# Performance work log

Measured on AMD Instinct MI355X. Metric: run time of the kernel, lower is better.

Reference implementation:

```python
import jax, jax.numpy as jnp
import numpy as np


def setup_inputs() -> dict:
    key = jax.random.key(0)
    ks = jax.random.split(key, 6)
    B, Q, K = 4, 512, 1024
    Dq, Dk, Dv, H = 512, 512, 512, 128
    return {
        "queries": jax.random.normal(ks[0], (B, Q, Dq), dtype=jnp.float32),
        "keys": jax.random.normal(ks[1], (B, K, Dk), dtype=jnp.float32),
        "values": jax.random.normal(ks[2], (B, K, Dv), dtype=jnp.float32),
        "W_q": jax.random.normal(ks[3], (Dq, H), dtype=jnp.float32) / np.sqrt(Dq),
        "W_k": jax.random.normal(ks[4], (Dk, H), dtype=jnp.float32) / np.sqrt(Dk),
        "w_v": jax.random.normal(ks[5], (H,), dtype=jnp.float32) / np.sqrt(H),
    }


def reference(queries, keys, values, W_q, W_k, w_v):
    # Additive (Bahdanau) attention.
    q = jnp.einsum("bqd,dh->bqh", queries, W_q)          # [B,Q,H]
    k = jnp.einsum("bkd,dh->bkh", keys, W_k)             # [B,K,H]
    features = jnp.tanh(q[:, :, None, :] + k[:, None, :, :])  # [B,Q,K,H]
    scores = jnp.einsum("bqkh,h->bqk", features, w_v)    # [B,Q,K]
    attn = jax.nn.softmax(scores, axis=-1)               # [B,Q,K]
    return jnp.einsum("bqk,bkv->bqv", attn, values)      # [B,Q,Dv]
```

## Files before the change

### kernel.cpp

```cpp
#include <hip/hip_runtime.h>

#define BB   4
#define QS   512
#define KSZ  1024
#define DD   512
#define HH   128
#define DVV  512
#define KPN  16

typedef unsigned int uint;
typedef unsigned short ushort;
typedef unsigned long long ull;
typedef __attribute__((ext_vector_type(8)))  short short8;
typedef __attribute__((ext_vector_type(16))) float f32x16;
typedef __attribute__((ext_vector_type(2)))  float f32x2;

__device__ __forceinline__ float rcp_fast(float x)  { return __builtin_amdgcn_rcpf(x); }
__device__ __forceinline__ float exp2_fast(float x) { return __builtin_amdgcn_exp2f(x); }
__device__ __forceinline__ f32x2 lo2(float4 v) { return (f32x2){v.x, v.y}; }
__device__ __forceinline__ f32x2 hi2(float4 v) { return (f32x2){v.z, v.w}; }

__device__ __forceinline__ void split1(float v, ushort& h, ushort& l) {
    uint u = __float_as_uint(v);
    h = (ushort)(u >> 16);
    float r = v - __uint_as_float(u & 0xffff0000u);
    l = (ushort)(__float_as_uint(r) >> 16);
}

__device__ __forceinline__ int hperm(int h) {
    return (h & ~3) | ((h & 1) << 1) | ((h >> 1) & 1);
}

#define NSQ  (BB * QS * DD / 4 / 256)
#define NSK  (BB * KSZ * DD / 4 / 256)
#define NWT  128
#define NPJ  192
#define NVT  (BB * (KSZ / 32) * (DVV / 32))

__global__ __launch_bounds__(256) void split_kernel(
    const float* __restrict__ q, const float* __restrict__ k,
    const float* __restrict__ Wq, const float* __restrict__ Wk,
    const float* __restrict__ wv, float* __restrict__ wvp,
    ushort* __restrict__ qh, ushort* __restrict__ ql,
    ushort* __restrict__ kh, ushort* __restrict__ kl,
    ushort* __restrict__ wqh, ushort* __restrict__ wql,
    ushort* __restrict__ wkh, ushort* __restrict__ wkl)
{
    const int id  = blockIdx.x;
    const int tid = threadIdx.x;

    if (id < NSQ + NSK) {
        const float* src; ushort* dh; ushort* dl; size_t i;
        if (id < NSQ) { src = q; dh = qh; dl = ql; i = (size_t)id * 256 + tid; }
        else          { src = k; dh = kh; dl = kl; i = (size_t)(id - NSQ) * 256 + tid; }
        float4 v = ((const float4*)src)[i];
        ushort h0,h1,h2,h3,l0,l1,l2,l3;
        split1(v.x,h0,l0); split1(v.y,h1,l1); split1(v.z,h2,l2); split1(v.w,h3,l3);
        *(ushort4*)&dh[i * 4] = make_ushort4(h0,h1,h2,h3);
        *(ushort4*)&dl[i * 4] = make_ushort4(l0,l1,l2,l3);
        return;
    }
    __shared__ float Ts[32][33];
    int t = id - (NSQ + NSK);
    if (t == 0 && tid < HH) wvp[hperm(tid)] = wv[tid];
    const float* W; ushort* dh; ushort* dl;
    if (t < 64) { W = Wq; dh = wqh; dl = wql; }
    else        { W = Wk; dh = wkh; dl = wkl; t -= 64; }
    const int d0 = (t >> 2) * 32, h0 = (t & 3) * 32;
    {
        const int dd = tid >> 3, c4 = (tid & 7) * 4;
        float4 v = *(const float4*)&W[(size_t)(d0 + dd) * HH + h0 + c4];
        Ts[dd][c4 + 0] = v.x; Ts[dd][c4 + 1] = v.y;
        Ts[dd][c4 + 2] = v.z; Ts[dd][c4 + 3] = v.w;
    }
    __syncthreads();
    {
        const int hh = tid >> 3, d4 = (tid & 7) * 4;
        ushort h[4], l[4];
        #pragma unroll
        for (int i = 0; i < 4; i++) split1(Ts[d4 + i][hh], h[i], l[i]);
        size_t o = (size_t)(h0 + hh) * DD + d0 + d4;
        *(ushort4*)&dh[o] = make_ushort4(h[0], h[1], h[2], h[3]);
        *(ushort4*)&dl[o] = make_ushort4(l[0], l[1], l[2], l[3]);
    }
}

__global__ __launch_bounds__(256) void projvt_kernel(
    const ushort* __restrict__ qh, const ushort* __restrict__ ql,
    const ushort* __restrict__ kh, const ushort* __restrict__ kl,
    const ushort* __restrict__ wqh, const ushort* __restrict__ wql,
    const ushort* __restrict__ wkh, const ushort* __restrict__ wkl,
    const float* __restrict__ val,
    float* __restrict__ eq, float* __restrict__ ek,
    ushort* __restrict__ vhi, ushort* __restrict__ vlo)
{
    const int id  = blockIdx.x;
    const int tid = threadIdx.x;

    if (id >= NPJ) {
        __shared__ float Ts[32][33];
        const int t   = id - NPJ;
        const int b   = t >> 9;
        const int rem = t & 511;
        const int k0  = (rem >> 4) * 32;
        const int n0  = (rem & 15) * 32;
        {
            const int kk = tid >> 3, n4 = (tid & 7) * 4;
            float4 v = *(const float4*)&val[((size_t)b * KSZ + k0 + kk) * DVV + n0 + n4];
            Ts[kk][n4 + 0] = v.x; Ts[kk][n4 + 1] = v.y;
            Ts[kk][n4 + 2] = v.z; Ts[kk][n4 + 3] = v.w;
        }
        __syncthreads();
        {
            const int nn = tid >> 3, k4 = (tid & 7) * 4;
            ushort h[4], l[4];
            #pragma unroll
            for (int i = 0; i < 4; i++) split1(Ts[k4 + i][nn], h[i], l[i]);
            size_t o = ((size_t)b * DVV + n0 + nn) * KSZ + k0 + k4;
            *(ushort4*)&vhi[o] = make_ushort4(h[0], h[1], h[2], h[3]);
            *(ushort4*)&vlo[o] = make_ushort4(l[0], l[1], l[2], l[3]);
        }
        return;
    }

    const int w = tid >> 6, lane = tid & 63;
    const int row = lane & 31, kg = lane >> 5;
    const int gw = id * 4 + w;

    const ushort *pa_h, *pa_l, *pb_h, *pb_l; float* op; int m0, nt;
    if (gw < 256) {
        m0 = (gw >> 2) * 32; nt = gw & 3;
        pa_h = qh; pa_l = ql; pb_h = wqh; pb_l = wql; op = eq;
    } else {
        const int g = gw - 256;
        m0 = (g >> 2) * 32; nt = g & 3;
        pa_h = kh; pa_l = kl; pb_h = wkh; pb_l = wkl; op = ek;
    }

    const ushort* ah_p = pa_h + (size_t)(m0 + row) * DD + kg * 8;
    const ushort* al_p = pa_l + (size_t)(m0 + row) * DD + kg * 8;
    const ushort* bh_p = pb_h + (size_t)(nt * 32 + row) * DD + kg * 8;
    const ushort* bl_p = pb_l + (size_t)(nt * 32 + row) * DD + kg * 8;

    f32x16 acc;
    #pragma unroll
    for (int i = 0; i < 16; i++) acc[i] = 0.f;

    #pragma unroll 8
    for (int ks = 0; ks < DD; ks += 16) {
        short8 ah = *(const short8*)(ah_p + ks);
        short8 al = *(const short8*)(al_p + ks);
        short8 bh = *(const short8*)(bh_p + ks);
        short8 bl = *(const short8*)(bl_p + ks);
        acc = __builtin_amdgcn_mfma_f32_32x32x16_bf16(ah, bh, acc, 0, 0, 0);
        acc = __builtin_amdgcn_mfma_f32_32x32x16_bf16(ah, bl, acc, 0, 0, 0);
        acc = __builtin_amdgcn_mfma_f32_32x32x16_bf16(al, bh, acc, 0, 0, 0);
    }

    const float C2L = 2.8853900817779268f;
    float* ob = op + (size_t)m0 * HH + nt * 32;
    const int prow = hperm(row);
    #pragma unroll
    for (int r = 0; r < 16; r++) {
        const int rb = (r & 3) + 8 * (r >> 2) + 4 * kg;
        ob[(size_t)rb * HH + prow] = fminf(exp2_fast(acc[r] * C2L), 5.0e4f);
    }
}

__global__ __launch_bounds__(256, 2) void spv_kernel(
    const float* __restrict__ eq, const float* __restrict__ ek,
    const float* __restrict__ wvp,
    const ushort* __restrict__ vhi, const ushort* __restrict__ vlo,
    float* __restrict__ opart, float* __restrict__ rsp)
{
    __shared__ float eqs[64][132];
    __shared__ float eks[64][132];
    ushort (*PhS)[68] = (ushort (*)[68])&eks[0][0];
    ushort (*PlS)[68] = (ushort (*)[68])((ushort*)&eks[0][0] + 64 * 68);

    const int id  = blockIdx.x;
    const int kp  = ((id >> 3) & 1) * 8 + (id & 7);
    const int b   = (id >> 4) & 3;
    const int qt  = id >> 6;

    const int tid  = threadIdx.x;
    const int w    = tid >> 6, lane = tid & 63;
    const int tq   = tid >> 4;
    const int tk   = tid & 15;
    const int wn   = w * 128;
    const int arow = lane & 31;
    const int akg  = lane >> 5;

    const float* eqg = eq + ((size_t)b * QS + qt * 64) * HH;
    const float* ekg = ek + ((size_t)b * KSZ + kp * 64) * HH;
    #pragma unroll
    for (int i = 0; i < 8; i++) {
        int f = tid + i * 256;
        *(float4*)&eqs[f >> 5][(f & 31) * 4] =
            *(const float4*)&eqg[(size_t)(f >> 5) * HH + (f & 31) * 4];
    }
    #pragma unroll
    for (int i = 0; i < 8; i++) {
        int f = tid + i * 256;
        *(float4*)&eks[f >> 5][(f & 31) * 4] =
            *(const float4*)&ekg[(size_t)(f >> 5) * HH + (f & 31) * 4];
    }
    __syncthreads();

    const f32x2 one2 = {1.0f, 1.0f};

#define SGROUP(eq4, ek4, sacc) { \
    f32x2 u02 = __builtin_elementwise_fma(lo2(eq4), lo2(ek4), one2); \
    f32x2 u13 = __builtin_elementwise_fma(hi2(eq4), hi2(ek4), one2); \
    f32x2 p_  = u02 * u13; \
    f32x2 n_  = __builtin_elementwise_fma(wA, u13, wB * u02); \
    float N_  = fmaf(n_.x, p_.y, n_.y * p_.x); \
    sacc = fmaf(N_, rcp_fast(p_.x * p_.y), sacc); }

    float s[4][4];
    #pragma unroll
    for (int a = 0; a < 4; a++)
        #pragma unroll
        for (int c = 0; c < 4; c++) s[a][c] = 0.f;

    #pragma unroll 4
    for (int h = 0; h < HH; h += 4) {
        float4 wp4 = *(const float4*)&wvp[h];
        f32x2 wA = lo2(wp4), wB = hi2(wp4);
        float4 eq4[4], ek4[4];
        #pragma unroll
        for (int a = 0; a < 4; a++) eq4[a] = *(const float4*)&eqs[tq + 16 * a][h];
        #pragma unroll
        for (int c = 0; c < 4; c++) ek4[c] = *(const float4*)&eks[tk + 16 * c][h];
        #pragma unroll
        for (int a = 0; a < 4; a++) {
            #pragma unroll
            for (int c = 0; c < 4; c++) SGROUP(eq4[a], ek4[c], s[a][c]);
        }
    }
#undef SGROUP

    const float CN = -2.8853900817779268f;
    float pv[4][4];
    ushort phv[4][4], plv[4][4];
    float rowacc[4] = {0.f, 0.f, 0.f, 0.f};
    #pragma unroll
    for (int a = 0; a < 4; a++) {
        #pragma unroll
        for (int c = 0; c < 4; c++) {
            pv[a][c] = exp2_fast(s[a][c] * CN);
            split1(pv[a][c], phv[a][c], plv[a][c]);
            rowacc[a] += pv[a][c];
        }
    }

    __syncthreads();

    #pragma unroll
    for (int a = 0; a < 4; a++) {
        #pragma unroll
        for (int c = 0; c < 4; c++) {
            PhS[tq + 16 * a][tk + 16 * c] = phv[a][c];
            PlS[tq + 16 * a][tk + 16 * c] = plv[a][c];
        }
    }

    #pragma unroll
    for (int m = 8; m; m >>= 1) {
        #pragma unroll
        for (int a = 0; a < 4; a++) rowacc[a] += __shfl_xor(rowacc[a], m);
    }
    if (tk == 0) {
        #pragma unroll
        for (int a = 0; a < 4; a++)
            rsp[((size_t)b * QS + qt * 64 + tq + 16 * a) * KPN + kp] = rowacc[a];
    }

    __syncthreads();

    f32x16 acc[2][4];
    #pragma unroll
    for (int hlf = 0; hlf < 2; hlf++)
        #pragma unroll
        for (int nb = 0; nb < 4; nb++)
            #pragma unroll
            for (int i = 0; i < 16; i++) acc[hlf][nb][i] = 0.f;

    const size_t vrow0 = ((size_t)b * DVV + wn + arow) * KSZ + kp * 64 + akg * 8;
    const ushort* vhb = vhi + vrow0;
    const ushort* vlb = vlo + vrow0;

    #pragma unroll
    for (int kb = 0; kb < 4; kb++) {
        short8 ah[2], al[2];
        #pragma unroll
        for (int hlf = 0; hlf < 2; hlf++) {
            { const ull* p = (const ull*)&PhS[hlf * 32 + arow][kb * 16 + akg * 8];
              ((ull*)&ah[hlf])[0] = p[0]; ((ull*)&ah[hlf])[1] = p[1]; }
            { const ull* p = (const ull*)&PlS[hlf * 32 + arow][kb * 16 + akg * 8];
              ((ull*)&al[hlf])[0] = p[0]; ((ull*)&al[hlf])[1] = p[1]; }
        }
        #pragma unroll
        for (int nb = 0; nb < 4; nb++) {
            const size_t o = (size_t)nb * 32 * KSZ + kb * 16;
            short8 vh = *(const short8*)(vhb + o);
            short8 vl = *(const short8*)(vlb + o);
            #pragma unroll
            for (int hlf = 0; hlf < 2; hlf++) {
                acc[hlf][nb] = __builtin_amdgcn_mfma_f32_32x32x16_bf16(ah[hlf], vh, acc[hlf][nb], 0, 0, 0);
                acc[hlf][nb] = __builtin_amdgcn_mfma_f32_32x32x16_bf16(ah[hlf], vl, acc[hlf][nb], 0, 0, 0);
                acc[hlf][nb] = __builtin_amdgcn_mfma_f32_32x32x16_bf16(al[hlf], vh, acc[hlf][nb], 0, 0, 0);
            }
        }
    }

    #pragma unroll
    for (int hlf = 0; hlf < 2; hlf++) {
        float* ob = opart + (((size_t)kp * BB + b) * QS + qt * 64 + hlf * 32) * DVV + wn;
        #pragma unroll
        for (int nb = 0; nb < 4; nb++) {
            #pragma unroll
            for (int r = 0; r < 16; r++) {
                const int rb = (r & 3) + 8 * (r >> 2) + 4 * akg;
                ob[(size_t)rb * DVV + nb * 32 + arow] = acc[hlf][nb][r];
            }
        }
    }
}

__global__ __launch_bounds__(256) void norm_kernel(
    const float* __restrict__ opart, const float* __restrict__ rsp,
    float* __restrict__ outp)
{
    const int i  = blockIdx.x * 256 + threadIdx.x;
    const int n4 = (i & 127) * 4;
    const int q  = (i >> 7) & (QS - 1);
    const int b  = i >> 16;

    const float* rp = rsp + ((size_t)b * QS + q) * KPN;
    float s = 0.f;
    #pragma unroll
    for (int j = 0; j < KPN / 4; j++) {
        float4 r = *(const float4*)(rp + j * 4);
        s += r.x + r.y + r.z + r.w;
    }
    float inv = rcp_fast(s);

    float ox = 0.f, oy = 0.f, oz = 0.f, ow = 0.f;
    #pragma unroll
    for (int kp = 0; kp < KPN; kp++) {
        float4 v = *(const float4*)&opart[(((size_t)kp * BB + b) * QS + q) * DVV + n4];
        ox += v.x; oy += v.y; oz += v.z; ow += v.w;
    }
    float4 res = make_float4(ox * inv, oy * inv, oz * inv, ow * inv);
    *(float4*)&outp[((size_t)b * QS + q) * DVV + n4] = res;
}

extern "C" void kernel_launch(void* const* d_in, const int* in_sizes, int n_in,
                              void* d_out, int out_size, void* d_ws, size_t ws_size,
                              hipStream_t stream)
{
    const float* queries = (const float*)d_in[0];
    const float* keys    = (const float*)d_in[1];
    const float* values  = (const float*)d_in[2];
    const float* Wq      = (const float*)d_in[3];
    const float* Wk      = (const float*)d_in[4];
    const float* wv      = (const float*)d_in[5];
    float* out = (float*)d_out;

    float*  eq    = (float*)d_ws;
    float*  ek    = eq  + (size_t)BB * QS * HH;
    float*  rsp   = ek  + (size_t)BB * KSZ * HH;
    float*  wvp   = rsp + (size_t)BB * QS * KPN;
    float*  opart = wvp + 256;
    ushort* vhi = (ushort*)(opart + (size_t)KPN * BB * QS * DVV);
    ushort* vlo = vhi + (size_t)BB * KSZ * DVV;
    ushort* qh  = vlo + (size_t)BB * KSZ * DVV;
    ushort* ql  = qh  + (size_t)BB * QS * DD;
    ushort* kh  = ql  + (size_t)BB * QS * DD;
    ushort* kl  = kh  + (size_t)BB * KSZ * DD;
    ushort* wqh = kl  + (size_t)BB * KSZ * DD;
    ushort* wql = wqh + (size_t)HH * DD;
    ushort* wkh = wql + (size_t)HH * DD;
    ushort* wkl = wkh + (size_t)HH * DD;

    split_kernel<<<dim3(NSQ + NSK + NWT), 256, 0, stream>>>(
        queries, keys, Wq, Wk, wv, wvp, qh, ql, kh, kl, wqh, wql, wkh, wkl);

    projvt_kernel<<<dim3(NPJ + NVT), 256, 0, stream>>>(
        qh, ql, kh, kl, wqh, wql, wkh, wkl, values, eq, ek, vhi, vlo);

    spv_kernel<<<dim3(512), 256, 0, stream>>>(eq, ek, wvp, vhi, vlo, opart, rsp);

    norm_kernel<<<dim3(1024), 256, 0, stream>>>(opart, rsp, out);
}
```

Before: 147.4 us.

## Halve spv query tile to 32 rows, doubling grid and raising occupancy

The fused score/softmax/PV kernel now processes 32 query rows per block instead of 64. That doubles the grid to 1024 blocks, drops the shared eq tile (queries are read straight from global memory), and raises the launch-bounds occupancy hint from 2 to 4. Each thread computes a 4x2 score tile instead of 4x4, and each wave issues one 32-row MFMA set instead of two. The aim is more waves in flight and less LDS per block. The cost is more global reloads of ek and V, since each V tile is now fetched twice as often, and less work per block over which to amortise loads.

```diff
diff --git a/kernel.cpp b/kernel.cpp
--- a/kernel.cpp
+++ b/kernel.cpp
@@ -167,38 +167,31 @@
     }
 }
 
-__global__ __launch_bounds__(256, 2) void spv_kernel(
+__global__ __launch_bounds__(256, 4) void spv_kernel(
     const float* __restrict__ eq, const float* __restrict__ ek,
     const float* __restrict__ wvp,
     const ushort* __restrict__ vhi, const ushort* __restrict__ vlo,
     float* __restrict__ opart, float* __restrict__ rsp)
 {
-    __shared__ float eqs[64][132];
     __shared__ float eks[64][132];
     ushort (*PhS)[68] = (ushort (*)[68])&eks[0][0];
-    ushort (*PlS)[68] = (ushort (*)[68])((ushort*)&eks[0][0] + 64 * 68);
+    ushort (*PlS)[68] = (ushort (*)[68])((ushort*)&eks[0][0] + 32 * 68);
 
     const int id  = blockIdx.x;
-    const int kp  = ((id >> 3) & 1) * 8 + (id & 7);
+    const int kp  = id & 15;
     const int b   = (id >> 4) & 3;
     const int qt  = id >> 6;
 
     const int tid  = threadIdx.x;
     const int w    = tid >> 6, lane = tid & 63;
-    const int tq   = tid >> 4;
-    const int tk   = tid & 15;
+    const int tq   = tid >> 5;
+    const int tk   = tid & 31;
     const int wn   = w * 128;
     const int arow = lane & 31;
     const int akg  = lane >> 5;
 
-    const float* eqg = eq + ((size_t)b * QS + qt * 64) * HH;
+    const float* eqg = eq + ((size_t)b * QS + qt * 32) * HH;
     const float* ekg = ek + ((size_t)b * KSZ + kp * 64) * HH;
-    #pragma unroll
-    for (int i = 0; i < 8; i++) {
-        int f = tid + i * 256;
-        *(float4*)&eqs[f >> 5][(f & 31) * 4] =
-            *(const float4*)&eqg[(size_t)(f >> 5) * HH + (f & 31) * 4];
-    }
     #pragma unroll
     for (int i = 0; i < 8; i++) {
         int f = tid + i * 256;
@@ -217,74 +210,74 @@
     float N_  = fmaf(n_.x, p_.y, n_.y * p_.x); \
     sacc = fmaf(N_, rcp_fast(p_.x * p_.y), sacc); }
 
-    float s[4][4];
-    #pragma unroll
-    for (int a = 0; a < 4; a++)
-        #pragma unroll
-        for (int c = 0; c < 4; c++) s[a][c] = 0.f;
+    float s[4][2];
+    #pragma unroll
+    for (int a = 0; a < 4; a++) { s[a][0] = 0.f; s[a][1] = 0.f; }
+
+    const float* eqr0 = eqg + (size_t)tq * HH;
+    const float* eqr1 = eqr0 + 8 * HH;
+    const float* eqr2 = eqr0 + 16 * HH;
+    const float* eqr3 = eqr0 + 24 * HH;
 
     #pragma unroll 4
     for (int h = 0; h < HH; h += 4) {
         float4 wp4 = *(const float4*)&wvp[h];
         f32x2 wA = lo2(wp4), wB = hi2(wp4);
-        float4 eq4[4], ek4[4];
-        #pragma unroll
-        for (int a = 0; a < 4; a++) eq4[a] = *(const float4*)&eqs[tq + 16 * a][h];
-        #pragma unroll
-        for (int c = 0; c < 4; c++) ek4[c] = *(const float4*)&eks[tk + 16 * c][h];
+        float4 eq4[4], ek4[2];
+        eq4[0] = *(const float4*)(eqr0 + h);
+        eq4[1] = *(const float4*)(eqr1 + h);
+        eq4[2] = *(const float4*)(eqr2 + h);
+        eq4[3] = *(const float4*)(eqr3 + h);
+        ek4[0] = *(const float4*)&eks[tk][h];
+        ek4[1] = *(const float4*)&eks[tk + 32][h];
         #pragma unroll
         for (int a = 0; a < 4; a++) {
-            #pragma unroll
-            for (int c = 0; c < 4; c++) SGROUP(eq4[a], ek4[c], s[a][c]);
+            SGROUP(eq4[a], ek4[0], s[a][0]);
+            SGROUP(eq4[a], ek4[1], s[a][1]);
         }
     }
 #undef SGROUP
 
     const float CN = -2.8853900817779268f;
-    float pv[4][4];
-    ushort phv[4][4], plv[4][4];
-    float rowacc[4] = {0.f, 0.f, 0.f, 0.f};
+    ushort phv[4][2], plv[4][2];
+    float rowacc[4];
     #pragma unroll
     for (int a = 0; a < 4; a++) {
-        #pragma unroll
-        for (int c = 0; c < 4; c++) {
-            pv[a][c] = exp2_fast(s[a][c] * CN);
-            split1(pv[a][c], phv[a][c], plv[a][c]);
-            rowacc[a] += pv[a][c];
-        }
+        float p0 = exp2_fast(s[a][0] * CN);
+        float p1 = exp2_fast(s[a][1] * CN);
+        split1(p0, phv[a][0], plv[a][0]);
+        split1(p1, phv[a][1], plv[a][1]);
+        rowacc[a] = p0 + p1;
     }
 
     __syncthreads();
 
     #pragma unroll
     for (int a = 0; a < 4; a++) {
-        #pragma unroll
-        for (int c = 0; c < 4; c++) {
-            PhS[tq + 16 * a][tk + 16 * c] = phv[a][c];
-            PlS[tq + 16 * a][tk + 16 * c] = plv[a][c];
-        }
-    }
-
-    #pragma unroll
-    for (int m = 8; m; m >>= 1) {
+        PhS[tq + 8 * a][tk]      = phv[a][0];
+        PlS[tq + 8 * a][tk]      = plv[a][0];
+        PhS[tq + 8 * a][tk + 32] = phv[a][1];
+        PlS[tq + 8 * a][tk + 32] = plv[a][1];
+    }
+
+    #pragma unroll
+    for (int m = 16; m; m >>= 1) {
         #pragma unroll
         for (int a = 0; a < 4; a++) rowacc[a] += __shfl_xor(rowacc[a], m);
     }
     if (tk == 0) {
         #pragma unroll
         for (int a = 0; a < 4; a++)
-            rsp[((size_t)b * QS + qt * 64 + tq + 16 * a) * KPN + kp] = rowacc[a];
+            rsp[((size_t)b * QS + qt * 32 + tq + 8 * a) * KPN + kp] = rowacc[a];
     }
 
     __syncthreads();
 
-    f32x16 acc[2][4];
-    #pragma unroll
-    for (int hlf = 0; hlf < 2; hlf++)
-        #pragma unroll
-        for (int nb = 0; nb < 4; nb++)
-            #pragma unroll
-            for (int i = 0; i < 16; i++) acc[hlf][nb][i] = 0.f;
+    f32x16 acc[4];
+    #pragma unroll
+    for (int nb = 0; nb < 4; nb++)
+        #pragma unroll
+        for (int i = 0; i < 16; i++) acc[nb][i] = 0.f;
 
     const size_t vrow0 = ((size_t)b * DVV + wn + arow) * KSZ + kp * 64 + akg * 8;
     const ushort* vhb = vhi + vrow0;
@@ -292,38 +285,29 @@
 
     #pragma unroll
     for (int kb = 0; kb < 4; kb++) {
-        short8 ah[2], al[2];
-        #pragma unroll
-        for (int hlf = 0; hlf < 2; hlf++) {
-            { const ull* p = (const ull*)&PhS[hlf * 32 + arow][kb * 16 + akg * 8];
-              ((ull*)&ah[hlf])[0] = p[0]; ((ull*)&ah[hlf])[1] = p[1]; }
-            { const ull* p = (const ull*)&PlS[hlf * 32 + arow][kb * 16 + akg * 8];
-              ((ull*)&al[hlf])[0] = p[0]; ((ull*)&al[hlf])[1] = p[1]; }
-        }
+        short8 ah, al;
+        { const ull* p = (const ull*)&PhS[arow][kb * 16 + akg * 8];
+          ((ull*)&ah)[0] = p[0]; ((ull*)&ah)[1] = p[1]; }
+        { const ull* p = (const ull*)&PlS[arow][kb * 16 + akg * 8];
+          ((ull*)&al)[0] = p[0]; ((ull*)&al)[1] = p[1]; }
         #pragma unroll
         for (int nb = 0; nb < 4; nb++) {
             const size_t o = (size_t)nb * 32 * KSZ + kb * 16;
             short8 vh = *(const short8*)(vhb + o);
             short8 vl = *(const short8*)(vlb + o);
-            #pragma unroll
-            for (int hlf = 0; hlf < 2; hlf++) {
-                acc[hlf][nb] = __builtin_amdgcn_mfma_f32_32x32x16_bf16(ah[hlf], vh, acc[hlf][nb], 0, 0, 0);
-                acc[hlf][nb] = __builtin_amdgcn_mfma_f32_32x32x16_bf16(ah[hlf], vl, acc[hlf][nb], 0, 0, 0);
-                acc[hlf][nb] = __builtin_amdgcn_mfma_f32_32x32x16_bf16(al[hlf], vh, acc[hlf][nb], 0, 0, 0);
-            }
-        }
-    }
-
-    #pragma unroll
-    for (int hlf = 0; hlf < 2; hlf++) {
-        float* ob = opart + (((size_t)kp * BB + b) * QS + qt * 64 + hlf * 32) * DVV + wn;
-        #pragma unroll
-        for (int nb = 0; nb < 4; nb++) {
-            #pragma unroll
-            for (int r = 0; r < 16; r++) {
-                const int rb = (r & 3) + 8 * (r >> 2) + 4 * akg;
-                ob[(size_t)rb * DVV + nb * 32 + arow] = acc[hlf][nb][r];
-            }
+            acc[nb] = __builtin_amdgcn_mfma_f32_32x32x16_bf16(ah, vh, acc[nb], 0, 0, 0);
+            acc[nb] = __builtin_amdgcn_mfma_f32_32x32x16_bf16(ah, vl, acc[nb], 0, 0, 0);
+            acc[nb] = __builtin_amdgcn_mfma_f32_32x32x16_bf16(al, vh, acc[nb], 0, 0, 0);
+        }
+    }
+
+    float* ob = opart + (((size_t)kp * BB + b) * QS + qt * 32) * DVV + wn;
+    #pragma unroll
+    for (int nb = 0; nb < 4; nb++) {
+        #pragma unroll
+        for (int r = 0; r < 16; r++) {
+            const int rb = (r & 3) + 8 * (r >> 2) + 4 * akg;
+            ob[(size_t)rb * DVV + nb * 32 + arow] = acc[nb][r];
         }
     }
 }
@@ -390,7 +374,7 @@
     projvt_kernel<<<dim3(NPJ + NVT), 256, 0, stream>>>(
         qh, ql, kh, kl, wqh, wql, wkh, wkl, values, eq, ek, vhi, vlo);
 
-    spv_kernel<<<dim3(512), 256, 0, stream>>>(eq, ek, wvp, vhi, vlo, opart, rsp);
+    spv_kernel<<<dim3(1024), 256, 0, stream>>>(eq, ek, wvp, vhi, vlo, opart, rsp);
 
     norm_kernel<<<dim3(1024), 256, 0, stream>>>(opart, rsp, out);
 }
```

After: 148.3 us. About the same (+0.6%).

## Split score and PV stages, materialize P in bf16 and fuse normalization

Applied to the files above, without the earlier changes.

The fused scores+PV kernel is split into a scores kernel that writes the softmax numerators as hi/lo bf16 planes to global memory, and a PV kernel that computes full-K products per output tile. The split-K partial outputs and the separate normalization pass are removed, and the final reduction and row scaling happen in LDS inside the PV kernel. This trades a large fp32 partial-sum round trip for a smaller bf16 P round trip. V is re-read per q-tile without LDS reuse.

```diff
diff --git a/kernel.cpp b/kernel.cpp
--- a/kernel.cpp
+++ b/kernel.cpp
@@ -167,29 +167,23 @@
     }
 }
 
-__global__ __launch_bounds__(256, 2) void spv_kernel(
+__global__ __launch_bounds__(256, 2) void scores_kernel(
     const float* __restrict__ eq, const float* __restrict__ ek,
     const float* __restrict__ wvp,
-    const ushort* __restrict__ vhi, const ushort* __restrict__ vlo,
-    float* __restrict__ opart, float* __restrict__ rsp)
+    ushort* __restrict__ Phi, ushort* __restrict__ Plo,
+    float* __restrict__ rsp)
 {
     __shared__ float eqs[64][132];
     __shared__ float eks[64][132];
-    ushort (*PhS)[68] = (ushort (*)[68])&eks[0][0];
-    ushort (*PlS)[68] = (ushort (*)[68])((ushort*)&eks[0][0] + 64 * 68);
 
     const int id  = blockIdx.x;
     const int kp  = ((id >> 3) & 1) * 8 + (id & 7);
     const int b   = (id >> 4) & 3;
     const int qt  = id >> 6;
 
-    const int tid  = threadIdx.x;
-    const int w    = tid >> 6, lane = tid & 63;
-    const int tq   = tid >> 4;
-    const int tk   = tid & 15;
-    const int wn   = w * 128;
-    const int arow = lane & 31;
-    const int akg  = lane >> 5;
+    const int tid = threadIdx.x;
+    const int tq  = tid >> 4;
+    const int tk  = tid & 15;
 
     const float* eqg = eq + ((size_t)b * QS + qt * 64) * HH;
     const float* ekg = ek + ((size_t)b * KSZ + kp * 64) * HH;
@@ -241,27 +235,19 @@
 #undef SGROUP
 
     const float CN = -2.8853900817779268f;
-    float pv[4][4];
-    ushort phv[4][4], plv[4][4];
+    ushort* ph = Phi + ((size_t)b * QS + qt * 64) * KSZ + kp * 64;
+    ushort* pl = Plo + ((size_t)b * QS + qt * 64) * KSZ + kp * 64;
     float rowacc[4] = {0.f, 0.f, 0.f, 0.f};
     #pragma unroll
     for (int a = 0; a < 4; a++) {
         #pragma unroll
         for (int c = 0; c < 4; c++) {
-            pv[a][c] = exp2_fast(s[a][c] * CN);
-            split1(pv[a][c], phv[a][c], plv[a][c]);
-            rowacc[a] += pv[a][c];
-        }
-    }
-
-    __syncthreads();
-
-    #pragma unroll
-    for (int a = 0; a < 4; a++) {
-        #pragma unroll
-        for (int c = 0; c < 4; c++) {
-            PhS[tq + 16 * a][tk + 16 * c] = phv[a][c];
-            PlS[tq + 16 * a][tk + 16 * c] = plv[a][c];
+            float p = exp2_fast(s[a][c] * CN);
+            ushort hh, ll;
+            split1(p, hh, ll);
+            size_t o = (size_t)(tq + 16 * a) * KSZ + tk + 16 * c;
+            ph[o] = hh; pl[o] = ll;
+            rowacc[a] += p;
         }
     }
 
@@ -275,85 +261,78 @@
         for (int a = 0; a < 4; a++)
             rsp[((size_t)b * QS + qt * 64 + tq + 16 * a) * KPN + kp] = rowacc[a];
     }
-
+}
+
+__global__ __launch_bounds__(256, 4) void pv_kernel(
+    const ushort* __restrict__ Phi, const ushort* __restrict__ Plo,
+    const ushort* __restrict__ vhi, const ushort* __restrict__ vlo,
+    const float* __restrict__ rsp, float* __restrict__ outp)
+{
+    __shared__ float red[4][32][33];
+    __shared__ float invS[32];
+
+    const int id = blockIdx.x;
+    const int ns = id & 15;
+    const int b  = (id >> 4) & 3;
+    const int qt = id >> 6;
+
+    const int tid = threadIdx.x, w = tid >> 6, lane = tid & 63;
+    const int arow = lane & 31;
+    const int akg  = lane >> 5;
+
+    if (tid < 32) {
+        const float* rp = rsp + ((size_t)b * QS + qt * 32 + tid) * KPN;
+        float s = 0.f;
+        #pragma unroll
+        for (int j = 0; j < KPN / 4; j++) {
+            float4 r = *(const float4*)(rp + j * 4);
+            s += r.x + r.y + r.z + r.w;
+        }
+        invS[tid] = rcp_fast(s);
+    }
+
+    f32x16 acc;
+    #pragma unroll
+    for (int i = 0; i < 16; i++) acc[i] = 0.f;
+
+    const size_t prow = ((size_t)b * QS + qt * 32 + arow) * KSZ + w * 256 + akg * 8;
+    const ushort* php = Phi + prow;
+    const ushort* plp = Plo + prow;
+    const size_t vrow = ((size_t)b * DVV + ns * 32 + arow) * KSZ + w * 256 + akg * 8;
+    const ushort* vhp = vhi + vrow;
+    const ushort* vlp = vlo + vrow;
+
+    #pragma unroll
+    for (int kb = 0; kb < 16; kb++) {
+        const size_t o = (size_t)kb * 16;
+        short8 ah = *(const short8*)(php + o);
+        short8 al = *(const short8*)(plp + o);
+        short8 vh = *(const short8*)(vhp + o);
+        short8 vl = *(const short8*)(vlp + o);
+        acc = __builtin_amdgcn_mfma_f32_32x32x16_bf16(ah, vh, acc, 0, 0, 0);
+        acc = __builtin_amdgcn_mfma_f32_32x32x16_bf16(ah, vl, acc, 0, 0, 0);
+        acc = __builtin_amdgcn_mfma_f32_32x32x16_bf16(al, vh, acc, 0, 0, 0);
+    }
+
+    #pragma unroll
+    for (int r = 0; r < 16; r++) {
+        const int rb = (r & 3) + 8 * (r >> 2) + 4 * akg;
+        red[w][rb][arow] = acc[r];
+    }
     __syncthreads();
 
-    f32x16 acc[2][4];
-    #pragma unroll
-    for (int hlf = 0; hlf < 2; hlf++)
-        #pragma unroll
-        for (int nb = 0; nb < 4; nb++)
-            #pragma unroll
-            for (int i = 0; i < 16; i++) acc[hlf][nb][i] = 0.f;
-
-    const size_t vrow0 = ((size_t)b * DVV + wn + arow) * KSZ + kp * 64 + akg * 8;
-    const ushort* vhb = vhi + vrow0;
-    const ushort* vlb = vlo + vrow0;
-
-    #pragma unroll
-    for (int kb = 0; kb < 4; kb++) {
-        short8 ah[2], al[2];
-        #pragma unroll
-        for (int hlf = 0; hlf < 2; hlf++) {
-            { const ull* p = (const ull*)&PhS[hlf * 32 + arow][kb * 16 + akg * 8];
-              ((ull*)&ah[hlf])[0] = p[0]; ((ull*)&ah[hlf])[1] = p[1]; }
-            { const ull* p = (const ull*)&PlS[hlf * 32 + arow][kb * 16 + akg * 8];
-              ((ull*)&al[hlf])[0] = p[0]; ((ull*)&al[hlf])[1] = p[1]; }
-        }
-        #pragma unroll
-        for (int nb = 0; nb < 4; nb++) {
-            const size_t o = (size_t)nb * 32 * KSZ + kb * 16;
-            short8 vh = *(const short8*)(vhb + o);
-            short8 vl = *(const short8*)(vlb + o);
-            #pragma unroll
-            for (int hlf = 0; hlf < 2; hlf++) {
-                acc[hlf][nb] = __builtin_amdgcn_mfma_f32_32x32x16_bf16(ah[hlf], vh, acc[hlf][nb], 0, 0, 0);
-                acc[hlf][nb] = __builtin_amdgcn_mfma_f32_32x32x16_bf16(ah[hlf], vl, acc[hlf][nb], 0, 0, 0);
-                acc[hlf][nb] = __builtin_amdgcn_mfma_f32_32x32x16_bf16(al[hlf], vh, acc[hlf][nb], 0, 0, 0);
-            }
-        }
-    }
-
-    #pragma unroll
-    for (int hlf = 0; hlf < 2; hlf++) {
-        float* ob = opart + (((size_t)kp * BB + b) * QS + qt * 64 + hlf * 32) * DVV + wn;
-        #pragma unroll
-        for (int nb = 0; nb < 4; nb++) {
-            #pragma unroll
-            for (int r = 0; r < 16; r++) {
-                const int rb = (r & 3) + 8 * (r >> 2) + 4 * akg;
-                ob[(size_t)rb * DVV + nb * 32 + arow] = acc[hlf][nb][r];
-            }
-        }
-    }
-}
-
-__global__ __launch_bounds__(256) void norm_kernel(
-    const float* __restrict__ opart, const float* __restrict__ rsp,
-    float* __restrict__ outp)
-{
-    const int i  = blockIdx.x * 256 + threadIdx.x;
-    const int n4 = (i & 127) * 4;
-    const int q  = (i >> 7) & (QS - 1);
-    const int b  = i >> 16;
-
-    const float* rp = rsp + ((size_t)b * QS + q) * KPN;
-    float s = 0.f;
-    #pragma unroll
-    for (int j = 0; j < KPN / 4; j++) {
-        float4 r = *(const float4*)(rp + j * 4);
-        s += r.x + r.y + r.z + r.w;
-    }
-    float inv = rcp_fast(s);
-
-    float ox = 0.f, oy = 0.f, oz = 0.f, ow = 0.f;
-    #pragma unroll
-    for (int kp = 0; kp < KPN; kp++) {
-        float4 v = *(const float4*)&opart[(((size_t)kp * BB + b) * QS + q) * DVV + n4];
-        ox += v.x; oy += v.y; oz += v.z; ow += v.w;
-    }
-    float4 res = make_float4(ox * inv, oy * inv, oz * inv, ow * inv);
-    *(float4*)&outp[((size_t)b * QS + q) * DVV + n4] = res;
+    const int q  = tid >> 3;
+    const int n4 = (tid & 7) * 4;
+    float4 s0 = *(const float4*)&red[0][q][n4];
+    float4 s1 = *(const float4*)&red[1][q][n4];
+    float4 s2 = *(const float4*)&red[2][q][n4];
+    float4 s3 = *(const float4*)&red[3][q][n4];
+    float inv = invS[q];
+    float4 res = make_float4((s0.x + s1.x + s2.x + s3.x) * inv,
+                             (s0.y + s1.y + s2.y + s3.y) * inv,
+                             (s0.z + s1.z + s2.z + s3.z) * inv,
+                             (s0.w + s1.w + s2.w + s3.w) * inv);
+    *(float4*)&outp[((size_t)b * QS + qt * 32 + q) * DVV + ns * 32 + n4] = res;
 }
 
 extern "C" void kernel_launch(void* const* d_in, const int* in_sizes, int n_in,
@@ -368,12 +347,13 @@
     const float* wv      = (const float*)d_in[5];
     float* out = (float*)d_out;
 
-    float*  eq    = (float*)d_ws;
-    float*  ek    = eq  + (size_t)BB * QS * HH;
-    float*  rsp   = ek  + (size_t)BB * KSZ * HH;
-    float*  wvp   = rsp + (size_t)BB * QS * KPN;
-    float*  opart = wvp + 256;
-    ushort* vhi = (ushort*)(opart + (size_t)KPN * BB * QS * DVV);
+    float*  eq  = (float*)d_ws;
+    float*  ek  = eq  + (size_t)BB * QS * HH;
+    float*  rsp = ek  + (size_t)BB * KSZ * HH;
+    float*  wvp = rsp + (size_t)BB * QS * KPN;
+    ushort* Phi = (ushort*)(wvp + 256);
+    ushort* Plo = Phi + (size_t)BB * QS * KSZ;
+    ushort* vhi = Plo + (size_t)BB * QS * KSZ;
     ushort* vlo = vhi + (size_t)BB * KSZ * DVV;
     ushort* qh  = vlo + (size_t)BB * KSZ * DVV;
     ushort* ql  = qh  + (size_t)BB * QS * DD;
@@ -390,7 +370,7 @@
     projvt_kernel<<<dim3(NPJ + NVT), 256, 0, stream>>>(
         qh, ql, kh, kl, wqh, wql, wkh, wkl, values, eq, ek, vhi, vlo);
 
-    spv_kernel<<<dim3(512), 256, 0, stream>>>(eq, ek, wvp, vhi, vlo, opart, rsp);
-
-    norm_kernel<<<dim3(1024), 256, 0, stream>>>(opart, rsp, out);
-}
+    scores_kernel<<<dim3(512), 256, 0, stream>>>(eq, ek, wvp, Phi, Plo, rsp);
+
+    pv_kernel<<<dim3(1024), 256, 0, stream>>>(Phi, Plo, vhi, vlo, rsp, out);
+}
```

New measurement: 162.4 us. 1.1x slower.
